# Kernel optimization log

Measured on AMD Instinct MI355X. Metric: run time of the kernel, lower is better.

## Reference

```python
import jax, jax.numpy as jnp
import numpy as np

B, S, HID = 2, 2048, 2304
H, KVH, D = 8, 4, 256          # query heads, kv heads, head_dim
N_REP = H // KVH
SCALE = 256.0 ** -0.5          # query_pre_attn_scalar ** -0.5
SOFTCAP = 50.0
ROPE_THETA = 10000.0
NEG = -1e9


def setup_inputs() -> dict:
    key = jax.random.key(0)
    k1, k2, k3, k4, k5 = jax.random.split(key, 5)
    hidden_states = jax.random.normal(k1, (B, S, HID), dtype=jnp.float32)
    # RoPE cos/sin tables, shape [B, S, D]
    inv_freq = 1.0 / (ROPE_THETA ** (jnp.arange(0, D, 2, dtype=jnp.float32) / D))
    pos = jnp.arange(S, dtype=jnp.float32)
    freqs = pos[:, None] * inv_freq[None, :]            # [S, D/2]
    emb = jnp.concatenate([freqs, freqs], axis=-1)      # [S, D]
    cos = jnp.broadcast_to(jnp.cos(emb)[None], (B, S, D))
    sin = jnp.broadcast_to(jnp.sin(emb)[None], (B, S, D))
    # additive causal mask [B, 1, S, S] (sliding_window=4096 > S, so pure causal)
    idx = jnp.arange(S)
    causal = idx[None, :] <= idx[:, None]
    attention_mask = jnp.broadcast_to(
        jnp.where(causal, 0.0, NEG).astype(jnp.float32)[None, None], (B, 1, S, S))
    # projection weights (lecun-normal-ish scale), no bias (attention_bias=False)
    Wq = jax.random.normal(k2, (HID, H * D), dtype=jnp.float32) / np.sqrt(HID)
    Wk = jax.random.normal(k3, (HID, KVH * D), dtype=jnp.float32) / np.sqrt(HID)
    Wv = jax.random.normal(k4, (HID, KVH * D), dtype=jnp.float32) / np.sqrt(HID)
    Wo = jax.random.normal(k5, (H * D, HID), dtype=jnp.float32) / np.sqrt(H * D)
    return {"hidden_states": hidden_states, "cos": cos, "sin": sin,
            "attention_mask": attention_mask,
            "Wq": Wq, "Wk": Wk, "Wv": Wv, "Wo": Wo}


def _rotate_half(x):
    half = x.shape[-1] // 2
    return jnp.concatenate([-x[..., half:], x[..., :half]], axis=-1)


def reference(hidden_states, cos, sin, attention_mask, Wq, Wk, Wv, Wo):
    b, s, _ = hidden_states.shape
    q = (hidden_states @ Wq).reshape(b, s, H, D).transpose(0, 2, 1, 3)    # [B,H,S,D]
    k = (hidden_states @ Wk).reshape(b, s, KVH, D).transpose(0, 2, 1, 3)  # [B,KVH,S,D]
    v = (hidden_states @ Wv).reshape(b, s, KVH, D).transpose(0, 2, 1, 3)
    c = cos[:, None]  # [B,1,S,D] broadcast over heads (unsqueeze_dim=1)
    sn = sin[:, None]
    q = q * c + _rotate_half(q) * sn
    k = k * c + _rotate_half(k) * sn
    # GQA: repeat kv heads (interleave, matching repeat_kv tile+reshape)
    k = jnp.repeat(k, N_REP, axis=1)
    v = jnp.repeat(v, N_REP, axis=1)
    w = jnp.einsum('bhqd,bhkd->bhqk', q, k) * SCALE
    w = jnp.tanh(w / SOFTCAP) * SOFTCAP                  # logit softcapping
    w = w + attention_mask[:, :, :, :s]
    w = jax.nn.softmax(w.astype(jnp.float32), axis=-1).astype(q.dtype)
    out = jnp.einsum('bhqk,bhkd->bhqd', w, v)
    out = out.transpose(0, 2, 1, 3).reshape(b, s, H * D)
    return out @ Wo
```

## Files before the change

### kernel.cpp

```cpp
#include <hip/hip_runtime.h>

typedef unsigned short u16;
typedef __attribute__((ext_vector_type(8))) short short8;
typedef __attribute__((ext_vector_type(4))) float f32x4;

constexpr int B_ = 2;
constexpr int H_ = 8;
constexpr int KVH_ = 4;
constexpr int S_ = 2048;
constexpr int D_ = 256;
constexpr int HID_ = 2304;
constexpr int QKVN_ = 4096;
constexpr int AON_ = 2048;

__device__ __forceinline__ float b2f(u16 u) {
  union { float f; unsigned int i; } x; x.i = ((unsigned int)u) << 16; return x.f;
}
__device__ __forceinline__ u16 f2b(float f) {
  unsigned int x = __float_as_uint(f);
  unsigned int r = (x + 0x7fffu + ((x >> 16) & 1u)) >> 16;
  return (u16)r;
}

__global__ void cast_kernel(const float* __restrict__ in, u16* __restrict__ out) {
  size_t i = ((size_t)blockIdx.x * 256 + threadIdx.x) * 4;
  float4 v = *(const float4*)(in + i);
  unsigned int lo = (unsigned int)f2b(v.x) | ((unsigned int)f2b(v.y) << 16);
  unsigned int hi = (unsigned int)f2b(v.z) | ((unsigned int)f2b(v.w) << 16);
  uint2 o; o.x = lo; o.y = hi;
  *(uint2*)(out + i) = o;
}

__global__ void transpose_cast_all(const float* __restrict__ s0, const float* __restrict__ s1,
                                   const float* __restrict__ s2, const float* __restrict__ s3,
                                   u16* __restrict__ d0, u16* __restrict__ d1,
                                   u16* __restrict__ d2, u16* __restrict__ d3) {
  __shared__ float tile[64][65];
  int which = blockIdx.z;
  const float* src; u16* dst; int R, C;
  if (which == 0)      { src = s0; dst = d0; R = 2304; C = 2048; }
  else if (which == 1) { src = s1; dst = d1; R = 2304; C = 1024; }
  else if (which == 2) { src = s2; dst = d2; R = 2304; C = 1024; }
  else                 { src = s3; dst = d3; R = 2048; C = 2304; }
  int r0 = blockIdx.y * 64, c0 = blockIdx.x * 64;
  if (r0 >= R || c0 >= C) return;
  int t = threadIdx.x;
#pragma unroll
  for (int i = 0; i < 16; ++i) {
    int e = i * 256 + t;
    int r = e >> 6, c = e & 63;
    tile[r][c] = src[(size_t)(r0 + r) * C + (c0 + c)];
  }
  __syncthreads();
#pragma unroll
  for (int i = 0; i < 16; ++i) {
    int e = i * 256 + t;
    int orow = e >> 6, ocol = e & 63;
    dst[(size_t)(c0 + orow) * R + (r0 + ocol)] = f2b(tile[ocol][orow]);
  }
}

template <int OUTF32>
__global__ __launch_bounds__(512, 2) void gemm_bt8(
    const u16* __restrict__ A, const u16* __restrict__ B, void* __restrict__ Cp,
    int M, int N, int K) {
  __shared__ u16 lds[2][2][2][8192];
  const int tid = threadIdx.x;
  const int lane = tid & 63;
  const int wave = tid >> 6;
  const int wm = wave >> 2, wn = wave & 3;
  const int quad = lane >> 4, l16 = lane & 15;
  const int m0 = blockIdx.y * 256, n0 = blockIdx.x * 256;
  const int nt = K >> 6;

  const int sub = tid >> 6;
  const int rr = (tid >> 2) & 15;
  const int cc = ((tid & 3) * 8) ^ ((rr & 8) ? 16 : 0);
  const int r_rel = (sub >> 1) * 16 + rr;
  const int ccol = (sub & 1) * 32 + cc;
  const u16* Asrc = A + (size_t)(m0 + r_rel) * K + ccol;
  const u16* Bsrc = B + (size_t)(n0 + r_rel) * K + ccol;
  const int ldsc = tid * 8;

  const int fr_off = l16 * 64 + (((quad * 8) ^ ((l16 & 8) ? 16 : 0)) << 1);

#define GL8(src, dst)                                                                  \
  __builtin_amdgcn_global_load_lds((const __attribute__((address_space(1))) void*)(src), \
                                   (__attribute__((address_space(3))) void*)(dst), 16, 0, 0)
#define STAGE_A(bf, kt, qp) {                                                          \
    const u16* _s = Asrc + (size_t)(kt) * 64;                                          \
    GL8(_s + (size_t)((qp) * 64) * K,       &lds[bf][0][0][(qp) * 4096 + ldsc]);       \
    GL8(_s + (size_t)(128 + (qp) * 64) * K, &lds[bf][0][1][(qp) * 4096 + ldsc]); }
#define STAGE_B(bf, kt, hf) {                                                          \
    const u16* _s = Bsrc + (size_t)(kt) * 64;                                          \
    GL8(_s + (size_t)((hf) * 128) * K,      &lds[bf][1][hf][ldsc]);                    \
    GL8(_s + (size_t)((hf) * 128 + 64) * K, &lds[bf][1][hf][4096 + ldsc]); }
#define LDA(bf, mi, kk) \
  (*(const short8*)((const char*)&lds[bf][0][wm][0] + (mi) * 2048 + (kk) * 1024 + fr_off))
#define LDB(bf, ni, kk) \
  (*(const short8*)((const char*)&lds[bf][1][wn >> 1][0] + ((wn & 1) * 4 + (ni)) * 2048 + (kk) * 1024 + fr_off))

  f32x4 acc[8][4] = {};
  short8 bfr[4][2], af[2][2];

  STAGE_B(0, 0, 0); STAGE_B(0, 0, 1); STAGE_A(0, 0, 0); STAGE_A(0, 0, 1);
  STAGE_B(1, 1, 0); STAGE_B(1, 1, 1); STAGE_A(1, 1, 0);
  asm volatile("s_waitcnt vmcnt(6)" ::: "memory");
  __builtin_amdgcn_s_barrier();

#define PHASE(q, STG, VMW)                                                             \
    _Pragma("unroll") for (int i = 0; i < 2; ++i)                                      \
      _Pragma("unroll") for (int kk = 0; kk < 2; ++kk) af[i][kk] = LDA(c, 2 * (q) + i, kk); \
    STG; VMW;                                                                          \
    __builtin_amdgcn_s_barrier();                                                      \
    asm volatile("s_waitcnt lgkmcnt(0)" ::: "memory");                                 \
    __builtin_amdgcn_sched_barrier(0);                                                 \
    __builtin_amdgcn_s_setprio(1);                                                     \
    _Pragma("unroll") for (int i = 0; i < 2; ++i)                                      \
      _Pragma("unroll") for (int ni = 0; ni < 4; ++ni)                                 \
        _Pragma("unroll") for (int kk = 0; kk < 2; ++kk)                               \
          acc[2 * (q) + i][ni] = __builtin_amdgcn_mfma_f32_16x16x32_bf16(              \
              af[i][kk], bfr[ni][kk], acc[2 * (q) + i][ni], 0, 0, 0);                  \
    __builtin_amdgcn_s_setprio(0);                                                     \
    __builtin_amdgcn_s_barrier();

  for (int T = 0; T < nt; ++T) {
    const int c = T & 1;
#pragma unroll
    for (int ni = 0; ni < 4; ++ni)
#pragma unroll
      for (int kk = 0; kk < 2; ++kk) bfr[ni][kk] = LDB(c, ni, kk);
    PHASE(0, if (T + 1 < nt) STAGE_A(c ^ 1, T + 1, 1), )
    PHASE(1, if (T + 2 < nt) STAGE_B(c, T + 2, 0), )
    PHASE(2, if (T + 2 < nt) STAGE_B(c, T + 2, 1), )
    PHASE(3, if (T + 2 < nt) STAGE_A(c, T + 2, 0),
          if (T + 2 >= nt) { asm volatile("s_waitcnt vmcnt(0)" ::: "memory"); }
          else             { asm volatile("s_waitcnt vmcnt(6)" ::: "memory"); })
  }
#undef PHASE
#undef LDA
#undef LDB
#undef STAGE_A
#undef STAGE_B
#undef GL8

#pragma unroll
  for (int mi = 0; mi < 8; ++mi) {
#pragma unroll
    for (int ni = 0; ni < 4; ++ni) {
#pragma unroll
      for (int r = 0; r < 4; ++r) {
        int row = m0 + wm * 128 + mi * 16 + quad * 4 + r;
        int col = n0 + wn * 64 + ni * 16 + l16;
        if (OUTF32)
          ((float*)Cp)[(size_t)row * N + col] = acc[mi][ni][r];
        else
          ((u16*)Cp)[(size_t)row * N + col] = f2b(acc[mi][ni][r]);
      }
    }
  }
}

__global__ void rope_kernel(const u16* __restrict__ qkv, const float* __restrict__ cs,
                            const float* __restrict__ sn, u16* __restrict__ Qr,
                            u16* __restrict__ Kr) {
  int row = blockIdx.x;
  int b = row >> 11, s = row & 2047;
  int d = threadIdx.x;
  const u16* qrow = qkv + (size_t)row * QKVN_;
  float c = cs[(size_t)row * D_ + d];
  float si = sn[(size_t)row * D_ + d];
  int dp = (d < 128) ? d + 128 : d - 128;
  float sgn = (d < 128) ? -1.f : 1.f;
#pragma unroll
  for (int h = 0; h < H_; ++h) {
    float v = b2f(qrow[h * D_ + d]);
    float p = sgn * b2f(qrow[h * D_ + dp]);
    Qr[((size_t)(b * H_ + h) * S_ + s) * D_ + d] = f2b(v * c + p * si);
  }
#pragma unroll
  for (int g = 0; g < KVH_; ++g) {
    float v = b2f(qrow[2048 + g * D_ + d]);
    float p = sgn * b2f(qrow[2048 + g * D_ + dp]);
    Kr[((size_t)(b * KVH_ + g) * S_ + s) * D_ + d] = f2b(v * c + p * si);
  }
}

__global__ void transpose_v(const u16* __restrict__ qkv, u16* __restrict__ Vt) {
  __shared__ u16 tile[64][72];
  int d0 = blockIdx.x * 64, s0 = blockIdx.y * 64, g = blockIdx.z;
  int b = g >> 2, kvh = g & 3;
  int t = threadIdx.x;
#pragma unroll
  for (int i = 0; i < 16; ++i) {
    int e = i * 256 + t;
    int r = e >> 6, c = e & 63;
    tile[r][c] = qkv[(size_t)(b * S_ + s0 + r) * QKVN_ + 3072 + kvh * D_ + d0 + c];
  }
  __syncthreads();
#pragma unroll
  for (int i = 0; i < 16; ++i) {
    int e = i * 256 + t;
    int orow = e >> 6, ocol = e & 63;
    Vt[((size_t)g * D_ + d0 + orow) * S_ + s0 + ocol] = tile[ocol][orow];
  }
}

__global__ __launch_bounds__(256, 2) void attn_kernel(
    const u16* __restrict__ Qr, const u16* __restrict__ Kr, const u16* __restrict__ Vt,
    float* __restrict__ Op0, float* __restrict__ Op1,
    float* __restrict__ Lp0, float* __restrict__ Lp1) {
  __shared__ u16 Ks[2][32 * 256];
  __shared__ u16 Vs[2][32 * 256];
  __shared__ u16 Ps[4][16 * 40];
  int u = blockIdx.x >> 1, sp = blockIdx.x & 1;
  int h = blockIdx.y;
  int kvh = h >> 1;
  int tid = threadIdx.x, wave = tid >> 6, lane = tid & 63;
  int quad = lane >> 4, l16 = lane & 15;
  float* Op = sp ? Op1 : Op0;
  float* Lp = sp ? Lp1 : Lp0;
  int ksrc_s[4], ksrc_c[4], vsrc_d[4], vsrc_s[4];
#pragma unroll
  for (int i = 0; i < 4; ++i) {
    int p = i * 256 + tid;
    ksrc_s[i] = p >> 5;
    ksrc_c[i] = (p & 31) ^ ((p >> 5) & 7);
    vsrc_d[i] = p >> 2;
    vsrc_s[i] = (p & 3) ^ ((p >> 3) & 3);
  }

  for (int part = 0; part < 2; ++part) {
    int b = part;
    int qt = (part == 0) ? u : (31 - u);
    int q0 = qt * 64;
    int beg = sp ? (qt + 1) : 0;
    int end = sp ? (2 * qt + 2) : (qt + 1);
    const u16* Qbase = Qr + ((size_t)(b * H_ + h) * S_ + q0 + wave * 16 + l16) * D_;
    short8 qf[8];
#pragma unroll
    for (int kk = 0; kk < 8; ++kk)
      qf[kk] = *(const short8*)(Qbase + kk * 32 + quad * 8);
    const u16* Kbase = Kr + (size_t)(b * KVH_ + kvh) * S_ * D_;
    const u16* Vbase = Vt + (size_t)(b * KVH_ + kvh) * D_ * S_;
    float lp[4] = {0.f, 0.f, 0.f, 0.f};
    f32x4 o_acc[16] = {};

#define STAGE(KT, BUF)                                                                   \
    {                                                                                    \
      int k0s = (KT) * 32;                                                               \
      _Pragma("unroll") for (int i = 0; i < 4; ++i) {                                    \
        int p = i * 256 + tid;                                                           \
        __builtin_amdgcn_global_load_lds(                                                \
            (const __attribute__((address_space(1))) void*)(Kbase +                      \
                (size_t)(k0s + ksrc_s[i]) * D_ + ksrc_c[i] * 8),                         \
            (__attribute__((address_space(3))) void*)(&Ks[BUF][0] + p * 8), 16, 0, 0);   \
      }                                                                                  \
      _Pragma("unroll") for (int i = 0; i < 4; ++i) {                                    \
        int p = i * 256 + tid;                                                           \
        __builtin_amdgcn_global_load_lds(                                                \
            (const __attribute__((address_space(1))) void*)(Vbase +                      \
                (size_t)vsrc_d[i] * S_ + k0s + vsrc_s[i] * 8),                           \
            (__attribute__((address_space(3))) void*)(&Vs[BUF][0] + p * 8), 16, 0, 0);   \
      }                                                                                  \
    }

    STAGE(beg, 0);
    __syncthreads();
    for (int kt = beg; kt < end; ++kt) {
      int k0 = kt * 32;
      int cur = (kt - beg) & 1;
      if (kt + 1 < end) STAGE(kt + 1, cur ^ 1);
      f32x4 sacc[2] = {};
#pragma unroll
      for (int n = 0; n < 2; ++n) {
        int srow = n * 16 + l16;
        const u16* kb = &Ks[cur][0] + srow * 256;
        int sw = l16 & 7;
#pragma unroll
        for (int kk = 0; kk < 8; ++kk) {
          int phys = (kk * 4 + quad) ^ sw;
          short8 bfr = *(const short8*)(kb + phys * 8);
          sacc[n] = __builtin_amdgcn_mfma_f32_16x16x32_bf16(qf[kk], bfr, sacc[n], 0, 0, 0);
        }
      }
      bool full = (k0 + 31 <= q0 + wave * 16);
#pragma unroll
      for (int n = 0; n < 2; ++n) {
        int key = k0 + n * 16 + l16;
#pragma unroll
        for (int r = 0; r < 4; ++r) {
          float E = __expf(sacc[n][r] * 0.0025f);
          float ee = __expf(-100.0f * __frcp_rn(E + 1.0f));
          if (!full) {
            int qq = q0 + wave * 16 + quad * 4 + r;
            ee = (key <= qq) ? ee : 0.0f;
          }
          lp[r] += ee;
          Ps[wave][(quad * 4 + r) * 40 + n * 16 + l16] = f2b(ee);
        }
      }
      short8 pa = *(const short8*)(&Ps[wave][l16 * 40 + quad * 8]);
#pragma unroll
      for (int dt = 0; dt < 16; ++dt) {
        int d = dt * 16 + l16;
        int phys = quad ^ ((d >> 1) & 3);
        short8 vb = *(const short8*)(&Vs[cur][0] + d * 32 + phys * 8);
        o_acc[dt] = __builtin_amdgcn_mfma_f32_16x16x32_bf16(pa, vb, o_acc[dt], 0, 0, 0);
      }
      __syncthreads();
    }
#undef STAGE
#pragma unroll
    for (int off = 1; off < 16; off <<= 1)
#pragma unroll
      for (int r = 0; r < 4; ++r)
        lp[r] += __shfl_xor(lp[r], off, 64);
    if (l16 == 0) {
#pragma unroll
      for (int r = 0; r < 4; ++r)
        Lp[((size_t)(b * H_ + h)) * S_ + q0 + wave * 16 + quad * 4 + r] = lp[r];
    }
#pragma unroll
    for (int dt = 0; dt < 16; ++dt)
#pragma unroll
      for (int r = 0; r < 4; ++r) {
        int row = b * S_ + q0 + wave * 16 + quad * 4 + r;
        int col = h * D_ + dt * 16 + l16;
        Op[(size_t)row * AON_ + col] = o_acc[dt][r];
      }
  }
}

__global__ void combine_kernel(const float* __restrict__ Op0, const float* __restrict__ Op1,
                               const float* __restrict__ Lp0, const float* __restrict__ Lp1,
                               u16* __restrict__ Ao) {
  size_t idx = (size_t)blockIdx.x * 256 + threadIdx.x;
  size_t row = idx >> 9;
  int c4 = ((int)idx & 511) * 4;
  const float4 a = *(const float4*)(Op0 + row * AON_ + c4);
  const float4 b4 = *(const float4*)(Op1 + row * AON_ + c4);
  int b = (int)(row >> 11), s = (int)row & 2047;
  int h = c4 >> 8;
  size_t li = ((size_t)(b * H_ + h)) * S_ + s;
  float inv = 1.0f / (Lp0[li] + Lp1[li]);
  unsigned int lo = (unsigned int)f2b((a.x + b4.x) * inv) | ((unsigned int)f2b((a.y + b4.y) * inv) << 16);
  unsigned int hi = (unsigned int)f2b((a.z + b4.z) * inv) | ((unsigned int)f2b((a.w + b4.w) * inv) << 16);
  uint2 o; o.x = lo; o.y = hi;
  *(uint2*)(Ao + row * AON_ + c4) = o;
}

extern "C" void kernel_launch(void* const* d_in, const int* in_sizes, int n_in,
                              void* d_out, int out_size, void* d_ws, size_t ws_size,
                              hipStream_t stream) {
  const float* hidden = (const float*)d_in[0];
  const float* cosp = (const float*)d_in[1];
  const float* sinp = (const float*)d_in[2];
  const float* Wq = (const float*)d_in[4];
  const float* Wk = (const float*)d_in[5];
  const float* Wv = (const float*)d_in[6];
  const float* Wo = (const float*)d_in[7];

  u16* hs  = (u16*)d_ws;
  u16* WT  = hs  + (size_t)4096 * HID_;
  u16* WoT = WT  + (size_t)4096 * HID_;
  u16* qkv = WoT + (size_t)HID_ * AON_;
  u16* Qr  = qkv + (size_t)4096 * QKVN_;
  u16* Kr  = Qr  + (size_t)B_ * H_ * S_ * D_;
  u16* Vt  = Kr  + (size_t)B_ * KVH_ * S_ * D_;
  u16* Ao  = Vt  + (size_t)B_ * KVH_ * S_ * D_;
  float* Lp0 = (float*)(Ao + (size_t)4096 * AON_);
  float* Lp1 = Lp0 + (size_t)B_ * H_ * S_;
  float* Op0 = (float*)hs;
  float* Op1 = (float*)qkv;

  cast_kernel<<<9216, 256, 0, stream>>>(hidden, hs);
  transpose_cast_all<<<dim3(36, 36, 4), 256, 0, stream>>>(
      Wq, Wk, Wv, Wo, WT, WT + (size_t)2048 * HID_, WT + (size_t)3072 * HID_, WoT);
  gemm_bt8<0><<<dim3(16, 16), 512, 0, stream>>>(hs, WT, qkv, 4096, QKVN_, HID_);
  rope_kernel<<<4096, 256, 0, stream>>>(qkv, cosp, sinp, Qr, Kr);
  transpose_v<<<dim3(4, 32, 8), 256, 0, stream>>>(qkv, Vt);
  attn_kernel<<<dim3(64, 8), 256, 0, stream>>>(Qr, Kr, Vt, Op0, Op1, Lp0, Lp1);
  combine_kernel<<<16384, 256, 0, stream>>>(Op0, Op1, Lp0, Lp1, Ao);
  gemm_bt8<1><<<dim3(9, 16), 512, 0, stream>>>(Ao, WoT, d_out, 4096, HID_, 2048);
}
```

Before: 410.7 us.

## Compute transposed S tile so P feeds PV MFMA from registers

Swaps the MFMA operand order to compute S^T, with K rows permuted and a new K-load swizzle, so each lane already holds the probabilities laid out as the A operand of the PV MFMA. This removes the per-tile shared-memory round trip through the Ps buffer and shrinks the row-sum reduction to two cross-lane shuffles. It also adds s_setprio around the MFMA blocks to favour matrix issue over other waves. The risk is a subtle layout or mask mismatch if the K row permutation does not line up with the key index used in the mask.

```diff
diff --git a/kernel.cpp b/kernel.cpp
--- a/kernel.cpp
+++ b/kernel.cpp
@@ -212,7 +212,6 @@
     float* __restrict__ Lp0, float* __restrict__ Lp1) {
   __shared__ u16 Ks[2][32 * 256];
   __shared__ u16 Vs[2][32 * 256];
-  __shared__ u16 Ps[4][16 * 40];
   int u = blockIdx.x >> 1, sp = blockIdx.x & 1;
   int h = blockIdx.y;
   int kvh = h >> 1;
@@ -224,11 +223,15 @@
 #pragma unroll
   for (int i = 0; i < 4; ++i) {
     int p = i * 256 + tid;
-    ksrc_s[i] = p >> 5;
-    ksrc_c[i] = (p & 31) ^ ((p >> 5) & 7);
+    int sK = p >> 5;
+    ksrc_s[i] = sK;
+    ksrc_c[i] = (p & 31) ^ ((sK & 3) | (((sK >> 3) & 1) << 2));
     vsrc_d[i] = p >> 2;
     vsrc_s[i] = (p & 3) ^ ((p >> 3) & 3);
   }
+  const int kg = l16 >> 2, ka = l16 & 3;
+  const int srow0 = 8 * kg + ka;
+  const int ksw = ka | ((kg & 1) << 2);
 
   for (int part = 0; part < 2; ++part) {
     int b = part;
@@ -243,8 +246,9 @@
       qf[kk] = *(const short8*)(Qbase + kk * 32 + quad * 8);
     const u16* Kbase = Kr + (size_t)(b * KVH_ + kvh) * S_ * D_;
     const u16* Vbase = Vt + (size_t)(b * KVH_ + kvh) * D_ * S_;
-    float lp[4] = {0.f, 0.f, 0.f, 0.f};
+    float lp = 0.f;
     f32x4 o_acc[16] = {};
+    const int qq = q0 + wave * 16 + l16;
 
 #define STAGE(KT, BUF)                                                                   \
     {                                                                                    \
@@ -272,35 +276,40 @@
       int cur = (kt - beg) & 1;
       if (kt + 1 < end) STAGE(kt + 1, cur ^ 1);
       f32x4 sacc[2] = {};
+      __builtin_amdgcn_s_setprio(1);
 #pragma unroll
       for (int n = 0; n < 2; ++n) {
-        int srow = n * 16 + l16;
-        const u16* kb = &Ks[cur][0] + srow * 256;
-        int sw = l16 & 7;
+        const u16* kb = &Ks[cur][0] + (srow0 + 4 * n) * 256;
 #pragma unroll
         for (int kk = 0; kk < 8; ++kk) {
-          int phys = (kk * 4 + quad) ^ sw;
-          short8 bfr = *(const short8*)(kb + phys * 8);
-          sacc[n] = __builtin_amdgcn_mfma_f32_16x16x32_bf16(qf[kk], bfr, sacc[n], 0, 0, 0);
+          int phys = (kk * 4 + quad) ^ ksw;
+          short8 kfr = *(const short8*)(kb + phys * 8);
+          sacc[n] = __builtin_amdgcn_mfma_f32_16x16x32_bf16(kfr, qf[kk], sacc[n], 0, 0, 0);
         }
       }
+      __builtin_amdgcn_s_setprio(0);
       bool full = (k0 + 31 <= q0 + wave * 16);
 #pragma unroll
       for (int n = 0; n < 2; ++n) {
-        int key = k0 + n * 16 + l16;
 #pragma unroll
         for (int r = 0; r < 4; ++r) {
           float E = __expf(sacc[n][r] * 0.0025f);
           float ee = __expf(-100.0f * __frcp_rn(E + 1.0f));
           if (!full) {
-            int qq = q0 + wave * 16 + quad * 4 + r;
+            int key = k0 + 8 * quad + 4 * n + r;
             ee = (key <= qq) ? ee : 0.0f;
           }
-          lp[r] += ee;
-          Ps[wave][(quad * 4 + r) * 40 + n * 16 + l16] = f2b(ee);
+          lp += ee;
+          sacc[n][r] = ee;
         }
       }
-      short8 pa = *(const short8*)(&Ps[wave][l16 * 40 + quad * 8]);
+      union { short8 s8; unsigned int d[4]; } pu;
+      pu.d[0] = (unsigned int)f2b(sacc[0][0]) | ((unsigned int)f2b(sacc[0][1]) << 16);
+      pu.d[1] = (unsigned int)f2b(sacc[0][2]) | ((unsigned int)f2b(sacc[0][3]) << 16);
+      pu.d[2] = (unsigned int)f2b(sacc[1][0]) | ((unsigned int)f2b(sacc[1][1]) << 16);
+      pu.d[3] = (unsigned int)f2b(sacc[1][2]) | ((unsigned int)f2b(sacc[1][3]) << 16);
+      short8 pa = pu.s8;
+      __builtin_amdgcn_s_setprio(1);
 #pragma unroll
       for (int dt = 0; dt < 16; ++dt) {
         int d = dt * 16 + l16;
@@ -308,19 +317,14 @@
         short8 vb = *(const short8*)(&Vs[cur][0] + d * 32 + phys * 8);
         o_acc[dt] = __builtin_amdgcn_mfma_f32_16x16x32_bf16(pa, vb, o_acc[dt], 0, 0, 0);
       }
+      __builtin_amdgcn_s_setprio(0);
       __syncthreads();
     }
 #undef STAGE
-#pragma unroll
-    for (int off = 1; off < 16; off <<= 1)
-#pragma unroll
-      for (int r = 0; r < 4; ++r)
-        lp[r] += __shfl_xor(lp[r], off, 64);
-    if (l16 == 0) {
-#pragma unroll
-      for (int r = 0; r < 4; ++r)
-        Lp[((size_t)(b * H_ + h)) * S_ + q0 + wave * 16 + quad * 4 + r] = lp[r];
-    }
+    lp += __shfl_xor(lp, 16, 64);
+    lp += __shfl_xor(lp, 32, 64);
+    if (lane < 16)
+      Lp[((size_t)(b * H_ + h)) * S_ + q0 + wave * 16 + lane] = lp;
 #pragma unroll
     for (int dt = 0; dt < 16; ++dt)
 #pragma unroll
```

Result: no change. 405.4 us (-1.3%).
